# Kernel tuning notes

Measured on AMD Instinct MI355X. Metric: run time of the kernel, lower is better.

The kernel has to match this reference:

```python
import jax, jax.numpy as jnp
import numpy as np

# Static module hyperparameters (from init_kwargs)
K = 4        # kernel_size
STRIDE = 2
L = 2        # n_layers
F = 4        # filters
NQ = 6       # n_qubits = ceil(log2(4*4*4)) = 6
D = 1 << NQ  # statevector dim = 64 = in_channels*K*K (no padding needed)

# Pauli-Z expectation sign table: wire 0 is the most-significant bit (PennyLane convention)
_bits = (jnp.arange(D)[None, :] >> (NQ - 1 - jnp.arange(NQ)[:, None])) & 1  # (NQ, D)
ZSIGNS = (1 - 2 * _bits).astype(jnp.float32)                                # (NQ, D)


def setup_inputs() -> dict:
    key = jax.random.key(0)
    k1, k2 = jax.random.split(key)
    x = jax.random.normal(k1, (128, 4, 64, 64), dtype=jnp.float32)
    weights = jax.random.normal(k2, (F, L, NQ, 3), dtype=jnp.float32)
    return {"x": x, "weights": weights}


def _rot_mat(phi, theta, omega):
    # qml.Rot = RZ(omega) @ RY(theta) @ RZ(phi)
    c = jnp.cos(theta / 2)
    s = jnp.sin(theta / 2)
    return jnp.stack([
        jnp.stack([jnp.exp(-1j * (phi + omega) / 2) * c, -jnp.exp(1j * (phi - omega) / 2) * s]),
        jnp.stack([jnp.exp(-1j * (phi - omega) / 2) * s, jnp.exp(1j * (phi + omega) / 2) * c]),
    ])  # (2,2) complex64


def _apply_1q(state, U, w):
    # state: (N, D) complex; apply 2x2 unitary on wire w (MSB-first ordering)
    N = state.shape[0]
    s = state.reshape(N, 1 << w, 2, 1 << (NQ - 1 - w))
    s = jnp.einsum('ij,najb->naib', U, s)
    return s.reshape(N, D)


def _apply_cnot(state, c, t):
    # flip target bit t where control bit c is 1
    N = state.shape[0]
    a, b = min(c, t), max(c, t)
    s = state.reshape(N, 1 << a, 2, 1 << (b - a - 1), 2, 1 << (NQ - 1 - b))
    if c < t:
        # control axis=2, target axis=4
        s = s.at[:, :, 1].set(s[:, :, 1, :, ::-1, :])
    else:
        # target axis=2, control axis=4
        s = s.at[:, :, :, :, 1, :].set(s[:, :, ::-1, :, 1, :])
    return s.reshape(N, D)


def _simulate(psi0, wf):
    # psi0: (N, D) complex64 normalized amplitudes; wf: (L, NQ, 3) float32
    state = psi0
    # The torch module applies StronglyEntanglingLayers(weights) L times -> L*L layers total.
    for _ in range(L):
        for l in range(L):
            for w in range(NQ):
                U = _rot_mat(wf[l, w, 0], wf[l, w, 1], wf[l, w, 2])
                state = _apply_1q(state, U, w)
            r = (l % (NQ - 1)) + 1  # StronglyEntanglingLayers default ranges
            for w in range(NQ):
                state = _apply_cnot(state, w, (w + r) % NQ)
    probs = state.real ** 2 + state.imag ** 2  # (N, D)
    return probs @ ZSIGNS.T                    # (N, NQ) Pauli-Z expvals


def reference(x, weights):
    B, C, H, W = x.shape
    oh = (H - K) // STRIDE + 1
    i = jnp.arange(oh) * STRIDE
    # vectorized sliding-window patch extraction, row-major (i outer, j inner)
    rows = x[:, :, i[:, None] + jnp.arange(K)[None, :], :]           # (B,C,oh,K,W)
    pat = rows[:, :, :, :, i[:, None] + jnp.arange(K)[None, :]]      # (B,C,oh,K,oh,K)
    pat = pat.transpose(0, 2, 4, 1, 3, 5).reshape(B, oh * oh, C * K * K)  # (B,P,D), flatten order (C,k,k)
    # AmplitudeEmbedding with normalize=True (C*K*K == 2**NQ, no padding)
    norm = jnp.linalg.norm(pat, axis=-1, keepdims=True)
    psi0 = (pat / norm).astype(jnp.complex64).reshape(-1, D)         # (B*P, D)
    exp = jax.vmap(lambda wf: _simulate(psi0, wf))(weights)          # (F, B*P, NQ)
    out = exp.reshape(F, B, oh * oh, NQ).transpose(1, 0, 3, 2).reshape(B, F * NQ, oh, oh)
    return out
```

## Files before the change

### kernel.cpp

```cpp
#include <hip/hip_runtime.h>

typedef float f32x2 __attribute__((ext_vector_type(2)));
typedef float f32x16 __attribute__((ext_vector_type(16)));
typedef __bf16 bf16x8 __attribute__((ext_vector_type(8)));

static __device__ __forceinline__ unsigned short f2bf(float v) {
    unsigned u = __builtin_bit_cast(unsigned, v);
    unsigned r = (u + 0x7FFFu + ((u >> 16) & 1u)) >> 16;
    return (unsigned short)r;
}
static __device__ __forceinline__ bf16x8 ldg8(const unsigned short* p) {
    uint4 u = *(const uint4*)p;
    return __builtin_bit_cast(bf16x8, u);
}
static __device__ __forceinline__ f32x16 mfma32(bf16x8 a, bf16x8 b, f32x16 c) {
    return __builtin_amdgcn_mfma_f32_32x32x16_bf16(a, b, c, 0, 0, 0);
}

static __device__ __forceinline__ float sum_xor32(float x) {
#if __has_builtin(__builtin_amdgcn_permlane32_swap)
    unsigned u = __builtin_bit_cast(unsigned, x);
    auto r = __builtin_amdgcn_permlane32_swap(u, u, false, false);
    return __builtin_bit_cast(float, (unsigned)r[0]) +
           __builtin_bit_cast(float, (unsigned)r[1]);
#else
    return x + __shfl_xor(x, 32);
#endif
}

__global__ __launch_bounds__(256) void prep_M(const float* __restrict__ wts,
                                              unsigned short* __restrict__ Mhi) {
    __shared__ float gls[12][8];
    const int f = blockIdx.x >> 4;
    const int tid = threadIdx.x;
    if (tid < 12) {
        int l = tid / 6, w = tid % 6;
        const float* p = wts + ((f * 2 + l) * 6 + w) * 3;
        float phi = p[0], theta = p[1], omega = p[2];
        float c, s; sincosf(0.5f * theta, &s, &c);
        float sapo, capo, samo, camo;
        sincosf(0.5f * (phi + omega), &sapo, &capo);
        sincosf(0.5f * (phi - omega), &samo, &camo);
        float* o = gls[tid];
        o[0] =  capo * c;  o[1] = -sapo * c;
        o[2] = -camo * s;  o[3] = -samo * s;
        o[4] =  camo * s;  o[5] = -samo * s;
        o[6] =  capo * c;  o[7] =  sapo * c;
    }
    __syncthreads();

    const int lane = tid & 63;
    const int wid  = tid >> 6;
    const int bas  = (blockIdx.x & 15) * 4 + wid;

    int src0 = lane, src1 = lane;
#pragma unroll
    for (int w = 5; w >= 0; --w) { int tq = (w + 1) % 6; src0 ^= ((src0 >> (5 - w)) & 1) << (5 - tq); }
#pragma unroll
    for (int w = 5; w >= 0; --w) { int tq = (w + 2) % 6; src1 ^= ((src1 >> (5 - w)) & 1) << (5 - tq); }

    float ar = (lane == bas) ? 1.0f : 0.0f, ai = 0.0f;
#pragma unroll
    for (int rep = 0; rep < 2; ++rep) {
#pragma unroll
        for (int l = 0; l < 2; ++l) {
#pragma unroll
            for (int w = 0; w < 6; ++w) {
                const float* gp = gls[l * 6 + w];
                const float4 uA = *(const float4*)gp;
                const float4 uB = *(const float4*)(gp + 4);
                const int m = 32 >> w;
                const float br = __shfl_xor(ar, m);
                const float bi = __shfl_xor(ai, m);
                const bool hi = (lane & m) != 0;
                const float cmr = hi ? uB.z : uA.x;
                const float cmi = hi ? uB.w : uA.y;
                const float cpr = hi ? uB.x : uA.z;
                const float cpi = hi ? uB.y : uA.w;
                const float nr = cmr * ar - cmi * ai + cpr * br - cpi * bi;
                const float ni = cmr * ai + cmi * ar + cpr * bi + cpi * br;
                ar = nr; ai = ni;
            }
            const int src = l ? src1 : src0;
            ar = __shfl(ar, src);
            ai = __shfl(ai, src);
        }
    }
    Mhi[((f * 2 + 0) * 64 + lane) * 64 + bas] = f2bf(ar);
    Mhi[((f * 2 + 1) * 64 + lane) * 64 + bas] = f2bf(ai);
}

__global__ __launch_bounds__(256, 3) void qconv_main(
        const float* __restrict__ x,
        const unsigned short* __restrict__ Mhi,
        float* __restrict__ out) {
    __shared__ __align__(16) unsigned short psiH[2][4096];
    __shared__ float zbuf[2][2][4][64][8];

    const int tid  = threadIdx.x;
    const int lane = tid & 63;
    const int w    = tid >> 6;
    const int bid  = blockIdx.x;

    {
        const int p = tid >> 2;
        const int q = tid & 3;
        const int n = bid * 64 + p;
        const int b0 = n / 961, pos = n - b0 * 961;
        const int i = pos / 31, j = pos - i * 31;
        const float* base0 = x + (((b0 * 4 + q) * 64) + i * 2) * 64 + j * 2;
        float v[2][16];
#pragma unroll
        for (int t = 0; t < 2; ++t) {
            const float* base = base0 + t * 64 * 4 * 64 * 64;
#pragma unroll
            for (int kh = 0; kh < 4; ++kh) {
                const float* r = base + kh * 64;
                *(f32x2*)&v[t][kh * 4]     = *(const f32x2*)r;
                *(f32x2*)&v[t][kh * 4 + 2] = *(const f32x2*)(r + 2);
            }
        }
#pragma unroll
        for (int t = 0; t < 2; ++t) {
            float ss = 0.f;
#pragma unroll
            for (int k = 0; k < 16; ++k) ss += v[t][k] * v[t][k];
            ss += __shfl_xor(ss, 1);
            ss += __shfl_xor(ss, 2);
            const float rn = rsqrtf(ss);
            unsigned hu[8];
#pragma unroll
            for (int k2 = 0; k2 < 8; ++k2) {
                __bf16 h0 = (__bf16)(v[t][2 * k2] * rn);
                __bf16 h1 = (__bf16)(v[t][2 * k2 + 1] * rn);
                hu[k2] = (unsigned)__builtin_bit_cast(unsigned short, h0)
                       | ((unsigned)__builtin_bit_cast(unsigned short, h1) << 16);
            }
            const int s0i = p * 64 + ((2 * q) ^ (p & 7)) * 8;
            const int s1i = p * 64 + ((2 * q + 1) ^ (p & 7)) * 8;
            *(uint4*)&psiH[t][s0i] = make_uint4(hu[0], hu[1], hu[2], hu[3]);
            *(uint4*)&psiH[t][s1i] = make_uint4(hu[4], hu[5], hu[6], hu[7]);
        }
    }

    const int hi5  = lane >> 5;
    const int arow = ((lane >> 4) & 1) * 4096 + (w * 16 + (lane & 15)) * 64 + hi5 * 8;

    bf16x8 A[4];
#pragma unroll
    for (int ks = 0; ks < 4; ++ks) A[ks] = ldg8(Mhi + arow + ks * 16);

    __syncthreads();

    bf16x8 Bh[2][2][4];
    const int pc = lane & 31;
#pragma unroll
    for (int t = 0; t < 2; ++t) {
#pragma unroll
        for (int ct = 0; ct < 2; ++ct) {
            const int pp = ct * 32 + pc;
#pragma unroll
            for (int ks = 0; ks < 4; ++ks) {
                const int idx = pp * 64 + ((2 * ks + hi5) ^ (pp & 7)) * 8;
                Bh[t][ct][ks] = __builtin_bit_cast(bf16x8, *(const uint4*)&psiH[t][idx]);
            }
        }
    }

#pragma unroll 1
    for (int f = 0; f < 4; ++f) {
        f32x16 C0, C1;
#pragma unroll
        for (int r = 0; r < 16; ++r) { C0[r] = 0.f; C1[r] = 0.f; }
#pragma unroll
        for (int ks = 0; ks < 4; ++ks) {
            C0 = mfma32(A[ks], Bh[0][0][ks], C0);
            C1 = mfma32(A[ks], Bh[0][1][ks], C1);
        }

        bf16x8 An[4];
        if (f < 3) {
#pragma unroll
            for (int ks = 0; ks < 4; ++ks)
                An[ks] = ldg8(Mhi + (f + 1) * 8192 + arow + ks * 16);
        }

#pragma unroll
        for (int t = 0; t < 2; ++t) {
            if (t == 1) {
#pragma unroll
                for (int r = 0; r < 16; ++r) { C0[r] = 0.f; C1[r] = 0.f; }
#pragma unroll
                for (int ks = 0; ks < 4; ++ks) {
                    C0 = mfma32(A[ks], Bh[1][0][ks], C0);
                    C1 = mfma32(A[ks], Bh[1][1][ks], C1);
                }
            }
#pragma unroll
            for (int ct = 0; ct < 2; ++ct) {
                const f32x16 Cv = ct ? C1 : C0;
                float P[8];
#pragma unroll
                for (int r = 0; r < 8; ++r) P[r] = Cv[r] * Cv[r] + Cv[r + 8] * Cv[r + 8];
                const float e0 = P[0] + P[1], o0 = P[0] - P[1];
                const float e1 = P[2] + P[3], o1 = P[2] - P[3];
                const float e2 = P[4] + P[5], o2 = P[4] - P[5];
                const float e3 = P[6] + P[7], o3 = P[6] - P[7];
                const float s01 = e0 + e1, s23 = e2 + e3;
                const float S = s01 + s23;
                const float Sr  = sum_xor32(S);
                const float Z2r = sum_xor32(s01 - s23);
                const float Z3r = sum_xor32(hi5 ? -S : S);
                const float Z4r = sum_xor32((e0 - e1) + (e2 - e3));
                const float Z5r = sum_xor32(o0 + o1 + o2 + o3);
                const int pp = ct * 32 + pc;
                float* zb = &zbuf[f & 1][t][w][pp][0];
                f32x2 d2;
                float d1;
                if (hi5 == 0) {
                    d2[0] = (w & 2) ? -Sr : Sr;
                    d2[1] = (w & 1) ? -Sr : Sr;
                    d1 = Z2r;
                } else {
                    d2[0] = Z3r;
                    d2[1] = Z4r;
                    d1 = Z5r;
                }
                *(f32x2*)(zb + hi5 * 4) = d2;
                zb[hi5 * 4 + 2] = d1;
            }
        }
        __syncthreads();

        {
            const int t    = tid >> 7;
            const int p    = (tid >> 1) & 63;
            const int half = tid & 1;
            float a0 = 0.f, a1 = 0.f, a2 = 0.f;
#pragma unroll
            for (int ww = 0; ww < 4; ++ww) {
                const float* zb = &zbuf[f & 1][t][ww][p][half * 4];
                const f32x2 v2 = *(const f32x2*)zb;
                a0 += v2[0]; a1 += v2[1]; a2 += zb[2];
            }
            const int nn = bid * 64 + p;
            int bb = nn / 961;
            const int pos = nn - bb * 961;
            bb += t * 64;
            float* o = out + (bb * 24 + f * 6 + half * 3) * 961 + pos;
            o[0]       = a0;
            o[961]     = a1;
            o[2 * 961] = a2;
        }

        if (f < 3) {
#pragma unroll
            for (int ks = 0; ks < 4; ++ks) A[ks] = An[ks];
        }
    }
}

extern "C" void kernel_launch(void* const* d_in, const int* in_sizes, int n_in,
                              void* d_out, int out_size, void* d_ws, size_t ws_size,
                              hipStream_t stream) {
    const float* x   = (const float*)d_in[0];
    const float* wts = (const float*)d_in[1];
    float* out = (float*)d_out;

    unsigned short* Mhi = (unsigned short*)d_ws;

    prep_M<<<64, 256, 0, stream>>>(wts, Mhi);

    qconv_main<<<961, 256, 0, stream>>>(x, Mhi, out);
}
```

Before: 29.81 us.

## Fuse matrix prep into main kernel with global flag synchronization

Merges the prep_M kernel into the main kernel: the first 64 blocks build the circuit unitary, write it to workspace and bump an atomic counter, while every block spins on that counter before loading the matrix. Patch loading and normalization now run before the wait, so they overlap the unitary build. This removes one kernel launch and its inter-kernel gap, but adds a memset launch and a spin-wait that relies on the first 64 blocks being scheduled. It also hoists the output address arithmetic out of the filter loop.

```diff
diff --git a/kernel.cpp b/kernel.cpp
--- a/kernel.cpp
+++ b/kernel.cpp
@@ -28,79 +28,80 @@
 #endif
 }
 
-__global__ __launch_bounds__(256) void prep_M(const float* __restrict__ wts,
-                                              unsigned short* __restrict__ Mhi) {
-    __shared__ float gls[12][8];
-    const int f = blockIdx.x >> 4;
-    const int tid = threadIdx.x;
-    if (tid < 12) {
-        int l = tid / 6, w = tid % 6;
-        const float* p = wts + ((f * 2 + l) * 6 + w) * 3;
-        float phi = p[0], theta = p[1], omega = p[2];
-        float c, s; sincosf(0.5f * theta, &s, &c);
-        float sapo, capo, samo, camo;
-        sincosf(0.5f * (phi + omega), &sapo, &capo);
-        sincosf(0.5f * (phi - omega), &samo, &camo);
-        float* o = gls[tid];
-        o[0] =  capo * c;  o[1] = -sapo * c;
-        o[2] = -camo * s;  o[3] = -samo * s;
-        o[4] =  camo * s;  o[5] = -samo * s;
-        o[6] =  capo * c;  o[7] =  sapo * c;
-    }
-    __syncthreads();
-
-    const int lane = tid & 63;
-    const int wid  = tid >> 6;
-    const int bas  = (blockIdx.x & 15) * 4 + wid;
-
-    int src0 = lane, src1 = lane;
-#pragma unroll
-    for (int w = 5; w >= 0; --w) { int tq = (w + 1) % 6; src0 ^= ((src0 >> (5 - w)) & 1) << (5 - tq); }
-#pragma unroll
-    for (int w = 5; w >= 0; --w) { int tq = (w + 2) % 6; src1 ^= ((src1 >> (5 - w)) & 1) << (5 - tq); }
-
-    float ar = (lane == bas) ? 1.0f : 0.0f, ai = 0.0f;
-#pragma unroll
-    for (int rep = 0; rep < 2; ++rep) {
-#pragma unroll
-        for (int l = 0; l < 2; ++l) {
-#pragma unroll
-            for (int w = 0; w < 6; ++w) {
-                const float* gp = gls[l * 6 + w];
-                const float4 uA = *(const float4*)gp;
-                const float4 uB = *(const float4*)(gp + 4);
-                const int m = 32 >> w;
-                const float br = __shfl_xor(ar, m);
-                const float bi = __shfl_xor(ai, m);
-                const bool hi = (lane & m) != 0;
-                const float cmr = hi ? uB.z : uA.x;
-                const float cmi = hi ? uB.w : uA.y;
-                const float cpr = hi ? uB.x : uA.z;
-                const float cpi = hi ? uB.y : uA.w;
-                const float nr = cmr * ar - cmi * ai + cpr * br - cpi * bi;
-                const float ni = cmr * ai + cmi * ar + cpr * bi + cpi * br;
-                ar = nr; ai = ni;
-            }
-            const int src = l ? src1 : src0;
-            ar = __shfl(ar, src);
-            ai = __shfl(ai, src);
-        }
-    }
-    Mhi[((f * 2 + 0) * 64 + lane) * 64 + bas] = f2bf(ar);
-    Mhi[((f * 2 + 1) * 64 + lane) * 64 + bas] = f2bf(ai);
-}
-
-__global__ __launch_bounds__(256, 3) void qconv_main(
+__global__ __launch_bounds__(256, 3) void qconv_fused(
         const float* __restrict__ x,
-        const unsigned short* __restrict__ Mhi,
+        const float* __restrict__ wts,
+        unsigned short* __restrict__ Mhi,
+        unsigned int* __restrict__ flag,
         float* __restrict__ out) {
     __shared__ __align__(16) unsigned short psiH[2][4096];
     __shared__ float zbuf[2][2][4][64][8];
+    __shared__ float gls[12][8];
 
     const int tid  = threadIdx.x;
     const int lane = tid & 63;
     const int w    = tid >> 6;
     const int bid  = blockIdx.x;
+
+    if (bid < 64) {
+        const int f = bid >> 4;
+        if (tid < 12) {
+            int l = tid / 6, ww = tid % 6;
+            const float* p = wts + ((f * 2 + l) * 6 + ww) * 3;
+            float phi = p[0], theta = p[1], omega = p[2];
+            float c, s; sincosf(0.5f * theta, &s, &c);
+            float sapo, capo, samo, camo;
+            sincosf(0.5f * (phi + omega), &sapo, &capo);
+            sincosf(0.5f * (phi - omega), &samo, &camo);
+            float* o = gls[tid];
+            o[0] =  capo * c;  o[1] = -sapo * c;
+            o[2] = -camo * s;  o[3] = -samo * s;
+            o[4] =  camo * s;  o[5] = -samo * s;
+            o[6] =  capo * c;  o[7] =  sapo * c;
+        }
+        __syncthreads();
+
+        const int bas = (bid & 15) * 4 + w;
+        int src0 = lane, src1 = lane;
+#pragma unroll
+        for (int g = 5; g >= 0; --g) { int tq = (g + 1) % 6; src0 ^= ((src0 >> (5 - g)) & 1) << (5 - tq); }
+#pragma unroll
+        for (int g = 5; g >= 0; --g) { int tq = (g + 2) % 6; src1 ^= ((src1 >> (5 - g)) & 1) << (5 - tq); }
+
+        float ar = (lane == bas) ? 1.0f : 0.0f, ai = 0.0f;
+#pragma unroll
+        for (int rep = 0; rep < 2; ++rep) {
+#pragma unroll
+            for (int l = 0; l < 2; ++l) {
+#pragma unroll
+                for (int g = 0; g < 6; ++g) {
+                    const float* gp = gls[l * 6 + g];
+                    const float4 uA = *(const float4*)gp;
+                    const float4 uB = *(const float4*)(gp + 4);
+                    const int m = 32 >> g;
+                    const float br = __shfl_xor(ar, m);
+                    const float bi = __shfl_xor(ai, m);
+                    const bool hi = (lane & m) != 0;
+                    const float cmr = hi ? uB.z : uA.x;
+                    const float cmi = hi ? uB.w : uA.y;
+                    const float cpr = hi ? uB.x : uA.z;
+                    const float cpi = hi ? uB.y : uA.w;
+                    const float nr = cmr * ar - cmi * ai + cpr * br - cpi * bi;
+                    const float ni = cmr * ai + cmi * ar + cpr * bi + cpi * br;
+                    ar = nr; ai = ni;
+                }
+                const int src = l ? src1 : src0;
+                ar = __shfl(ar, src);
+                ai = __shfl(ai, src);
+            }
+        }
+        Mhi[((f * 2 + 0) * 64 + lane) * 64 + bas] = f2bf(ar);
+        Mhi[((f * 2 + 1) * 64 + lane) * 64 + bas] = f2bf(ai);
+        __threadfence();
+        __syncthreads();
+        if (tid == 0)
+            __hip_atomic_fetch_add(flag, 1u, __ATOMIC_RELEASE, __HIP_MEMORY_SCOPE_AGENT);
+    }
 
     {
         const int p = tid >> 2;
@@ -142,18 +143,11 @@
             *(uint4*)&psiH[t][s1i] = make_uint4(hu[4], hu[5], hu[6], hu[7]);
         }
     }
-
-    const int hi5  = lane >> 5;
-    const int arow = ((lane >> 4) & 1) * 4096 + (w * 16 + (lane & 15)) * 64 + hi5 * 8;
-
-    bf16x8 A[4];
-#pragma unroll
-    for (int ks = 0; ks < 4; ++ks) A[ks] = ldg8(Mhi + arow + ks * 16);
-
     __syncthreads();
 
     bf16x8 Bh[2][2][4];
-    const int pc = lane & 31;
+    const int hi5 = lane >> 5;
+    const int pc  = lane & 31;
 #pragma unroll
     for (int t = 0; t < 2; ++t) {
 #pragma unroll
@@ -166,6 +160,26 @@
             }
         }
     }
+
+    if (tid == 0) {
+        while (__hip_atomic_load(flag, __ATOMIC_ACQUIRE, __HIP_MEMORY_SCOPE_AGENT) < 64u)
+            __builtin_amdgcn_s_sleep(8);
+    }
+    __syncthreads();
+
+    const int arow = ((lane >> 4) & 1) * 4096 + (w * 16 + (lane & 15)) * 64 + hi5 * 8;
+
+    bf16x8 A[4];
+#pragma unroll
+    for (int ks = 0; ks < 4; ++ks) A[ks] = ldg8(Mhi + arow + ks * 16);
+
+    const int ctile = tid >> 7;
+    const int cp    = (tid >> 1) & 63;
+    const int chalf = tid & 1;
+    const int cnn   = bid * 64 + cp;
+    const int cbb   = cnn / 961;
+    const int cpos  = cnn - cbb * 961;
+    float* const obase = out + (((cbb + ctile * 64) * 24) + chalf * 3) * 961 + cpos;
 
 #pragma unroll 1
     for (int f = 0; f < 4; ++f) {
@@ -233,21 +247,14 @@
         __syncthreads();
 
         {
-            const int t    = tid >> 7;
-            const int p    = (tid >> 1) & 63;
-            const int half = tid & 1;
             float a0 = 0.f, a1 = 0.f, a2 = 0.f;
 #pragma unroll
             for (int ww = 0; ww < 4; ++ww) {
-                const float* zb = &zbuf[f & 1][t][ww][p][half * 4];
+                const float* zb = &zbuf[f & 1][ctile][ww][cp][chalf * 4];
                 const f32x2 v2 = *(const f32x2*)zb;
                 a0 += v2[0]; a1 += v2[1]; a2 += zb[2];
             }
-            const int nn = bid * 64 + p;
-            int bb = nn / 961;
-            const int pos = nn - bb * 961;
-            bb += t * 64;
-            float* o = out + (bb * 24 + f * 6 + half * 3) * 961 + pos;
+            float* o = obase + f * 6 * 961;
             o[0]       = a0;
             o[961]     = a1;
             o[2 * 961] = a2;
@@ -268,8 +275,9 @@
     float* out = (float*)d_out;
 
     unsigned short* Mhi = (unsigned short*)d_ws;
-
-    prep_M<<<64, 256, 0, stream>>>(wts, Mhi);
-
-    qconv_main<<<961, 256, 0, stream>>>(x, Mhi, out);
-}
+    unsigned int*   flg = (unsigned int*)((char*)d_ws + 65536);
+
+    hipMemsetAsync(flg, 0, 4, stream);
+
+    qconv_fused<<<961, 256, 0, stream>>>(x, wts, Mhi, flg, out);
+}
```

Measured after the change: 72.81 us. +144.3%, slower.

## Double block to 512 threads, splitting batch halves across wave groups

Applied to the files above, without the earlier changes.

The main kernel now runs 512 threads per block. Each group of four waves handles one of the two batch halves, where before every wave processed both halves in sequence. The zbuf double-buffer across f is removed and replaced with an extra barrier per iteration. The final reduction now writes outputs coalesced, one element per thread, in place of three strided writes per thread. More threads per block halve the MFMA and epilogue work per wave and raise parallelism, at the cost of an extra __syncthreads per filter and more pressure on registers and occupancy.

```diff
diff --git a/kernel.cpp b/kernel.cpp
--- a/kernel.cpp
+++ b/kernel.cpp
@@ -90,61 +90,57 @@
     Mhi[((f * 2 + 1) * 64 + lane) * 64 + bas] = f2bf(ai);
 }
 
-__global__ __launch_bounds__(256, 3) void qconv_main(
+__global__ __launch_bounds__(512, 8) void qconv_main(
         const float* __restrict__ x,
         const unsigned short* __restrict__ Mhi,
         float* __restrict__ out) {
     __shared__ __align__(16) unsigned short psiH[2][4096];
-    __shared__ float zbuf[2][2][4][64][8];
+    __shared__ float zbuf[2][4][64][8];
 
     const int tid  = threadIdx.x;
     const int lane = tid & 63;
-    const int w    = tid >> 6;
+    const int w8   = tid >> 6;
+    const int dq   = w8 & 3;
+    const int tw   = w8 >> 2;
     const int bid  = blockIdx.x;
 
     {
-        const int p = tid >> 2;
+        const int t = tid >> 8;
+        const int p = (tid >> 2) & 63;
         const int q = tid & 3;
         const int n = bid * 64 + p;
         const int b0 = n / 961, pos = n - b0 * 961;
         const int i = pos / 31, j = pos - i * 31;
-        const float* base0 = x + (((b0 * 4 + q) * 64) + i * 2) * 64 + j * 2;
-        float v[2][16];
-#pragma unroll
-        for (int t = 0; t < 2; ++t) {
-            const float* base = base0 + t * 64 * 4 * 64 * 64;
-#pragma unroll
-            for (int kh = 0; kh < 4; ++kh) {
-                const float* r = base + kh * 64;
-                *(f32x2*)&v[t][kh * 4]     = *(const f32x2*)r;
-                *(f32x2*)&v[t][kh * 4 + 2] = *(const f32x2*)(r + 2);
-            }
-        }
-#pragma unroll
-        for (int t = 0; t < 2; ++t) {
-            float ss = 0.f;
-#pragma unroll
-            for (int k = 0; k < 16; ++k) ss += v[t][k] * v[t][k];
-            ss += __shfl_xor(ss, 1);
-            ss += __shfl_xor(ss, 2);
-            const float rn = rsqrtf(ss);
-            unsigned hu[8];
-#pragma unroll
-            for (int k2 = 0; k2 < 8; ++k2) {
-                __bf16 h0 = (__bf16)(v[t][2 * k2] * rn);
-                __bf16 h1 = (__bf16)(v[t][2 * k2 + 1] * rn);
-                hu[k2] = (unsigned)__builtin_bit_cast(unsigned short, h0)
-                       | ((unsigned)__builtin_bit_cast(unsigned short, h1) << 16);
-            }
-            const int s0i = p * 64 + ((2 * q) ^ (p & 7)) * 8;
-            const int s1i = p * 64 + ((2 * q + 1) ^ (p & 7)) * 8;
-            *(uint4*)&psiH[t][s0i] = make_uint4(hu[0], hu[1], hu[2], hu[3]);
-            *(uint4*)&psiH[t][s1i] = make_uint4(hu[4], hu[5], hu[6], hu[7]);
-        }
+        const float* base = x + ((((b0 + t * 64) * 4 + q) * 64) + i * 2) * 64 + j * 2;
+        float v[16];
+#pragma unroll
+        for (int kh = 0; kh < 4; ++kh) {
+            const float* r = base + kh * 64;
+            *(f32x2*)&v[kh * 4]     = *(const f32x2*)r;
+            *(f32x2*)&v[kh * 4 + 2] = *(const f32x2*)(r + 2);
+        }
+        float ss = 0.f;
+#pragma unroll
+        for (int k = 0; k < 16; ++k) ss += v[k] * v[k];
+        ss += __shfl_xor(ss, 1);
+        ss += __shfl_xor(ss, 2);
+        const float rn = rsqrtf(ss);
+        unsigned hu[8];
+#pragma unroll
+        for (int k2 = 0; k2 < 8; ++k2) {
+            __bf16 h0 = (__bf16)(v[2 * k2] * rn);
+            __bf16 h1 = (__bf16)(v[2 * k2 + 1] * rn);
+            hu[k2] = (unsigned)__builtin_bit_cast(unsigned short, h0)
+                   | ((unsigned)__builtin_bit_cast(unsigned short, h1) << 16);
+        }
+        const int s0i = p * 64 + ((2 * q) ^ (p & 7)) * 8;
+        const int s1i = p * 64 + ((2 * q + 1) ^ (p & 7)) * 8;
+        *(uint4*)&psiH[t][s0i] = make_uint4(hu[0], hu[1], hu[2], hu[3]);
+        *(uint4*)&psiH[t][s1i] = make_uint4(hu[4], hu[5], hu[6], hu[7]);
     }
 
     const int hi5  = lane >> 5;
-    const int arow = ((lane >> 4) & 1) * 4096 + (w * 16 + (lane & 15)) * 64 + hi5 * 8;
+    const int arow = ((lane >> 4) & 1) * 4096 + (dq * 16 + (lane & 15)) * 64 + hi5 * 8;
 
     bf16x8 A[4];
 #pragma unroll
@@ -152,20 +148,20 @@
 
     __syncthreads();
 
-    bf16x8 Bh[2][2][4];
+    bf16x8 Bh[2][4];
     const int pc = lane & 31;
 #pragma unroll
-    for (int t = 0; t < 2; ++t) {
-#pragma unroll
-        for (int ct = 0; ct < 2; ++ct) {
-            const int pp = ct * 32 + pc;
-#pragma unroll
-            for (int ks = 0; ks < 4; ++ks) {
-                const int idx = pp * 64 + ((2 * ks + hi5) ^ (pp & 7)) * 8;
-                Bh[t][ct][ks] = __builtin_bit_cast(bf16x8, *(const uint4*)&psiH[t][idx]);
-            }
-        }
-    }
+    for (int ct = 0; ct < 2; ++ct) {
+        const int pp = ct * 32 + pc;
+#pragma unroll
+        for (int ks = 0; ks < 4; ++ks) {
+            const int idx = pp * 64 + ((2 * ks + hi5) ^ (pp & 7)) * 8;
+            Bh[ct][ks] = __builtin_bit_cast(bf16x8, *(const uint4*)&psiH[tw][idx]);
+        }
+    }
+
+    const int cnn  = bid * 64 + (tid & 63);
+    (void)cnn;
 
 #pragma unroll 1
     for (int f = 0; f < 4; ++f) {
@@ -174,8 +170,8 @@
         for (int r = 0; r < 16; ++r) { C0[r] = 0.f; C1[r] = 0.f; }
 #pragma unroll
         for (int ks = 0; ks < 4; ++ks) {
-            C0 = mfma32(A[ks], Bh[0][0][ks], C0);
-            C1 = mfma32(A[ks], Bh[0][1][ks], C1);
+            C0 = mfma32(A[ks], Bh[0][ks], C0);
+            C1 = mfma32(A[ks], Bh[1][ks], C1);
         }
 
         bf16x8 An[4];
@@ -186,74 +182,57 @@
         }
 
 #pragma unroll
-        for (int t = 0; t < 2; ++t) {
-            if (t == 1) {
-#pragma unroll
-                for (int r = 0; r < 16; ++r) { C0[r] = 0.f; C1[r] = 0.f; }
-#pragma unroll
-                for (int ks = 0; ks < 4; ++ks) {
-                    C0 = mfma32(A[ks], Bh[1][0][ks], C0);
-                    C1 = mfma32(A[ks], Bh[1][1][ks], C1);
-                }
+        for (int ct = 0; ct < 2; ++ct) {
+            const f32x16 Cv = ct ? C1 : C0;
+            float P[8];
+#pragma unroll
+            for (int r = 0; r < 8; ++r) P[r] = Cv[r] * Cv[r] + Cv[r + 8] * Cv[r + 8];
+            const float e0 = P[0] + P[1], o0 = P[0] - P[1];
+            const float e1 = P[2] + P[3], o1 = P[2] - P[3];
+            const float e2 = P[4] + P[5], o2 = P[4] - P[5];
+            const float e3 = P[6] + P[7], o3 = P[6] - P[7];
+            const float s01 = e0 + e1, s23 = e2 + e3;
+            const float S = s01 + s23;
+            const float Sr  = sum_xor32(S);
+            const float Z2r = sum_xor32(s01 - s23);
+            const float Z3r = sum_xor32(hi5 ? -S : S);
+            const float Z4r = sum_xor32((e0 - e1) + (e2 - e3));
+            const float Z5r = sum_xor32(o0 + o1 + o2 + o3);
+            const int pp = ct * 32 + pc;
+            float* zb = &zbuf[tw][dq][pp][0];
+            f32x2 d2;
+            float d1;
+            if (hi5 == 0) {
+                d2[0] = (dq & 2) ? -Sr : Sr;
+                d2[1] = (dq & 1) ? -Sr : Sr;
+                d1 = Z2r;
+            } else {
+                d2[0] = Z3r;
+                d2[1] = Z4r;
+                d1 = Z5r;
             }
-#pragma unroll
-            for (int ct = 0; ct < 2; ++ct) {
-                const f32x16 Cv = ct ? C1 : C0;
-                float P[8];
-#pragma unroll
-                for (int r = 0; r < 8; ++r) P[r] = Cv[r] * Cv[r] + Cv[r + 8] * Cv[r + 8];
-                const float e0 = P[0] + P[1], o0 = P[0] - P[1];
-                const float e1 = P[2] + P[3], o1 = P[2] - P[3];
-                const float e2 = P[4] + P[5], o2 = P[4] - P[5];
-                const float e3 = P[6] + P[7], o3 = P[6] - P[7];
-                const float s01 = e0 + e1, s23 = e2 + e3;
-                const float S = s01 + s23;
-                const float Sr  = sum_xor32(S);
-                const float Z2r = sum_xor32(s01 - s23);
-                const float Z3r = sum_xor32(hi5 ? -S : S);
-                const float Z4r = sum_xor32((e0 - e1) + (e2 - e3));
-                const float Z5r = sum_xor32(o0 + o1 + o2 + o3);
-                const int pp = ct * 32 + pc;
-                float* zb = &zbuf[f & 1][t][w][pp][0];
-                f32x2 d2;
-                float d1;
-                if (hi5 == 0) {
-                    d2[0] = (w & 2) ? -Sr : Sr;
-                    d2[1] = (w & 1) ? -Sr : Sr;
-                    d1 = Z2r;
-                } else {
-                    d2[0] = Z3r;
-                    d2[1] = Z4r;
-                    d1 = Z5r;
-                }
-                *(f32x2*)(zb + hi5 * 4) = d2;
-                zb[hi5 * 4 + 2] = d1;
-            }
+            *(f32x2*)(zb + hi5 * 4) = d2;
+            zb[hi5 * 4 + 2] = d1;
         }
         __syncthreads();
 
-        {
-            const int t    = tid >> 7;
-            const int p    = (tid >> 1) & 63;
-            const int half = tid & 1;
-            float a0 = 0.f, a1 = 0.f, a2 = 0.f;
-#pragma unroll
-            for (int ww = 0; ww < 4; ++ww) {
-                const float* zb = &zbuf[f & 1][t][ww][p][half * 4];
-                const f32x2 v2 = *(const f32x2*)zb;
-                a0 += v2[0]; a1 += v2[1]; a2 += zb[2];
-            }
+#pragma unroll 1
+        for (int u = tid; u < 768; u += 512) {
+            const int t   = u / 384;
+            const int rem = u - t * 384;
+            const int q   = rem >> 6;
+            const int p   = rem & 63;
+            const int slot = q + (q >= 3);
+            const float* zb = &zbuf[t][0][p][slot];
+            const float sum = zb[0] + zb[512] + zb[1024] + zb[1536];
             const int nn = bid * 64 + p;
-            int bb = nn / 961;
+            const int bb = nn / 961;
             const int pos = nn - bb * 961;
-            bb += t * 64;
-            float* o = out + (bb * 24 + f * 6 + half * 3) * 961 + pos;
-            o[0]       = a0;
-            o[961]     = a1;
-            o[2 * 961] = a2;
+            out[((bb + t * 64) * 24 + f * 6 + q) * 961 + pos] = sum;
         }
 
         if (f < 3) {
+            __syncthreads();
 #pragma unroll
             for (int ks = 0; ks < 4; ++ks) A[ks] = An[ks];
         }
@@ -271,5 +250,5 @@
 
     prep_M<<<64, 256, 0, stream>>>(wts, Mhi);
 
-    qconv_main<<<961, 256, 0, stream>>>(x, Mhi, out);
-}
+    qconv_main<<<961, 512, 0, stream>>>(x, Mhi, out);
+}
```

New measurement: 92.25 us. 3.09x slower.
